# Optimization experiments

Hardware: AMD Instinct MI355X
Metric: run time of the kernel (lower is better)

The kernel has to match this reference:

```python
import jax, jax.numpy as jnp
import numpy as np

L, N, E, H = 4096, 1, 1024, 16
DH = E // H
SCALE = DH ** -0.5


def setup_inputs() -> dict:
    key = jax.random.key(0)
    k1, k2, k3 = jax.random.split(key, 3)
    # xavier_uniform-ish scales for faithfulness of magnitude
    lim_qkv = (6.0 / (3 * E + E)) ** 0.5
    lim_out = (6.0 / (E + E)) ** 0.5
    x = jax.random.normal(k1, (L, N, E), dtype=jnp.float32)
    w_qkv = jax.random.uniform(k2, (3 * E, E), dtype=jnp.float32, minval=-lim_qkv, maxval=lim_qkv)
    w_out = jax.random.uniform(k3, (E, E), dtype=jnp.float32, minval=-lim_out, maxval=lim_out)
    return {"x": x, "w_qkv": w_qkv, "w_out": w_out}


def reference(x, w_qkv, w_out):
    # x: [L, N, E]
    qkv = jnp.einsum('lne,fe->lnf', x, w_qkv)          # [L, N, 3E]
    q, k, v = jnp.split(qkv, 3, axis=-1)               # each [L, N, E]

    def to_heads(t):
        # [L, N, E] -> [N*H, L, DH]
        return t.reshape(L, N * H, DH).transpose(1, 0, 2)

    q = to_heads(q) * SCALE
    k = to_heads(k)
    v = to_heads(v)
    attn = jnp.einsum('bld,bmd->blm', q, k)            # [N*H, L, L]
    attn = jax.nn.softmax(attn, axis=-1)
    out = jnp.einsum('blm,bmd->bld', attn, v)          # [N*H, L, DH]
    out = out.transpose(1, 0, 2).reshape(L, N, E)
    return jnp.einsum('lne,fe->lnf', out, w_out)       # [L, N, E]
```

## Files before the change

### kernel.cpp

```cpp
#include <hip/hip_runtime.h>
#include <hip/hip_bf16.h>
#include <stdint.h>

#define L_SEQ 4096
#define EMB   1024
#define NHEAD 16
#define DHEAD 64

#define SM_SCALE 0.18033688011112042f
#define SM_FIXED_MAX 12.0f

typedef __attribute__((ext_vector_type(8))) short short8;
typedef __attribute__((ext_vector_type(4))) short s16x4;
typedef __attribute__((ext_vector_type(4))) float f32x4;

struct Pack8 { f32x4 lo, hi; };

__device__ inline short f2bf(float f) {
  union { float f; unsigned u; } c; c.f = f;
  unsigned r = (c.u + 0x7fffu + ((c.u >> 16) & 1u)) >> 16;
  return (short)(unsigned short)r;
}
__device__ inline unsigned fbits(float f) {
  union { float f; unsigned u; } c; c.f = f; return c.u;
}
__device__ inline unsigned pack_trunc(float f0, float f1) {
#if __has_builtin(__builtin_amdgcn_perm)
  return __builtin_amdgcn_perm(fbits(f1), fbits(f0), 0x07060302u);
#else
  return (fbits(f0) >> 16) | (fbits(f1) & 0xffff0000u);
#endif
}

#if __has_builtin(__builtin_amdgcn_exp2f)
#define EXP2F(x) __builtin_amdgcn_exp2f(x)
#else
#define EXP2F(x) exp2f(x)
#endif

__device__ inline void pl16swap(unsigned &x, unsigned &y) {
#if __has_builtin(__builtin_amdgcn_permlane16_swap)
  auto r = __builtin_amdgcn_permlane16_swap(x, y, false, false);
  x = r[0]; y = r[1];
#else
  asm volatile("v_permlane16_swap_b32 %0, %1" : "+v"(x), "+v"(y));
#endif
}

__device__ inline short8 mk8(unsigned d0, unsigned d1, unsigned d2, unsigned d3) {
  union { unsigned u[4]; short8 s; } c;
  c.u[0] = d0; c.u[1] = d1; c.u[2] = d2; c.u[3] = d3;
  return c.s;
}

template<bool F32>
__device__ inline auto ld8(const void* p, size_t off) {
  if constexpr (F32) {
    const float* f = (const float*)p + off;
    Pack8 r; r.lo = *(const f32x4*)f; r.hi = *(const f32x4*)(f + 4);
    return r;
  } else {
    return *(const short8*)((const short*)p + off);
  }
}
__device__ inline short8 cvt8(Pack8 r) {
  short8 o;
#pragma unroll
  for (int j = 0; j < 4; ++j) { o[j] = f2bf(r.lo[j]); o[4 + j] = f2bf(r.hi[j]); }
  return o;
}
__device__ inline short8 cvt8(short8 r) { return r; }

#define MFMA16(a, b, c) __builtin_amdgcn_mfma_f32_16x16x32_bf16(a, b, c, 0, 0, 0)
#define FZERO ((f32x4){0.f, 0.f, 0.f, 0.f})

__device__ inline void stage16(const void* g, void* l) {
  __builtin_amdgcn_global_load_lds(
      (const __attribute__((address_space(1))) void*)g,
      (__attribute__((address_space(3))) void*)l, 16, 0, 0);
}

__global__ __launch_bounds__(256)
void conv_kernel(const float* __restrict__ in, short* __restrict__ out, int n) {
  int i = (blockIdx.x * 256 + threadIdx.x) * 8;
  if (i >= n) return;
  Pack8 r; r.lo = *(const f32x4*)(in + i); r.hi = *(const f32x4*)(in + i + 4);
  *(short8*)(out + i) = cvt8(r);
}

__global__ __launch_bounds__(256, 3)
void gemm_qkv_dma(const short* __restrict__ A, const short* __restrict__ B,
                  short* __restrict__ qb, short* __restrict__ kb,
                  short* __restrict__ vt) {
  __shared__ __align__(16) short At[128 * 32];
  __shared__ __align__(16) short Bt[128 * 32];

  const int tid  = threadIdx.x;
  const int lane = tid & 63;
  const int wave = tid >> 6;
  const int quad = lane >> 4;
  const int l15  = lane & 15;
  const int q8   = quad << 3;

  const int bm  = (blockIdx.x / 24) << 7;
  const int bn  = (blockIdx.x % 24) << 7;
  const int wr  = wave >> 1;
  const int wc  = wave & 1;

  const short* Ab = A + (size_t)bm * EMB;
  const short* Bb = B + (size_t)bn * EMB;

  f32x4 acc[4][4];
#pragma unroll
  for (int r = 0; r < 4; ++r)
#pragma unroll
    for (int c = 0; c < 4; ++c) acc[r][c] = FZERO;

  const int arow = (wr * 64 + l15) * 32 + q8;
  const int brow = (wc * 64 + l15) * 32 + q8;
  const int wbase = tid & ~63;

  for (int kt = 0; kt < 32; ++kt) {
    __syncthreads();
    const int k0 = kt << 5;
#pragma unroll
    for (int j = 0; j < 2; ++j) {
      const int s = j * 256 + tid;
      const int row = s >> 2, qc = (s & 3) << 3;
      stage16(Ab + (size_t)row * EMB + k0 + qc,
              At + (size_t)(j * 256 + wbase) * 8);
      stage16(Bb + (size_t)row * EMB + k0 + qc,
              Bt + (size_t)(j * 256 + wbase) * 8);
    }
    __syncthreads();

    short8 af[4], bf[4];
#pragma unroll
    for (int r = 0; r < 4; ++r) af[r] = *(const short8*)(At + arow + r * 512);
#pragma unroll
    for (int c = 0; c < 4; ++c) bf[c] = *(const short8*)(Bt + brow + c * 512);
#pragma unroll
    for (int r = 0; r < 4; ++r)
#pragma unroll
      for (int c = 0; c < 4; ++c)
        acc[r][c] = MFMA16(af[r], bf[c], acc[r][c]);
  }

  if (bn < 2048) {
    short* dst = (bn < 1024) ? qb : kb;
    const int bcol = (bn < 1024) ? bn : bn - 1024;
    const float cs = (bn < 1024) ? SM_SCALE : 1.0f;
#pragma unroll
    for (int r = 0; r < 4; ++r)
#pragma unroll
      for (int c = 0; c < 4; ++c) {
        const int col = bcol + wc * 64 + c * 16 + l15;
#pragma unroll
        for (int reg = 0; reg < 4; ++reg) {
          const int row = bm + wr * 64 + r * 16 + quad * 4 + reg;
          dst[(size_t)row * EMB + col] = f2bf(acc[r][c][reg] * cs);
        }
      }
  } else {
    const int bcol = bn - 2048;
#pragma unroll
    for (int r = 0; r < 4; ++r)
#pragma unroll
      for (int c = 0; c < 4; ++c) {
        const int col  = bcol + wc * 64 + c * 16 + l15;
        const int rowb = bm + wr * 64 + r * 16 + quad * 4;
        s16x4 pk;
#pragma unroll
        for (int reg = 0; reg < 4; ++reg) pk[reg] = f2bf(acc[r][c][reg]);
        *(s16x4*)(vt + (size_t)col * L_SEQ + rowb) = pk;
      }
  }
}

__global__ __launch_bounds__(256, 3)
void gemm_qkv_f32(const short* __restrict__ A, const float* __restrict__ B,
                  short* __restrict__ qb, short* __restrict__ kb,
                  short* __restrict__ vt) {
  __shared__ __align__(16) short At[128 * 40];
  __shared__ __align__(16) short Bt[128 * 40];

  const int tid  = threadIdx.x;
  const int lane = tid & 63;
  const int wave = tid >> 6;
  const int quad = lane >> 4;
  const int l15  = lane & 15;
  const int q8   = quad << 3;

  const int bm  = (blockIdx.x / 24) << 7;
  const int bn  = (blockIdx.x % 24) << 7;
  const int wr  = wave >> 1;
  const int wc  = wave & 1;

  const int s0 = tid, s1 = tid + 256;
  const int ar0 = s0 >> 2, ac0 = (s0 & 3) << 3;
  const int ar1 = s1 >> 2, ac1 = (s1 & 3) << 3;

  const size_t aoff0 = (size_t)(bm + ar0) * EMB + ac0;
  const size_t aoff1 = (size_t)(bm + ar1) * EMB + ac1;
  const size_t boff0 = (size_t)(bn + ar0) * EMB + ac0;
  const size_t boff1 = (size_t)(bn + ar1) * EMB + ac1;

  f32x4 acc[4][4];
#pragma unroll
  for (int r = 0; r < 4; ++r)
#pragma unroll
    for (int c = 0; c < 4; ++c) acc[r][c] = FZERO;

  short8 ga0 = *(const short8*)(A + aoff0);
  short8 ga1 = *(const short8*)(A + aoff1);
  Pack8  gb0 = ld8<true>(B, boff0);
  Pack8  gb1 = ld8<true>(B, boff1);

  const int arow = (wr * 64 + l15) * 40 + q8;
  const int brow = (wc * 64 + l15) * 40 + q8;

  for (int kt = 0; kt < 32; ++kt) {
    __syncthreads();
    *(short8*)(At + ar0 * 40 + ac0) = ga0;
    *(short8*)(At + ar1 * 40 + ac1) = ga1;
    *(short8*)(Bt + ar0 * 40 + ac0) = cvt8(gb0);
    *(short8*)(Bt + ar1 * 40 + ac1) = cvt8(gb1);
    __syncthreads();

    if (kt + 1 < 32) {
      const size_t k0 = (size_t)(kt + 1) << 5;
      ga0 = *(const short8*)(A + aoff0 + k0);
      ga1 = *(const short8*)(A + aoff1 + k0);
      gb0 = ld8<true>(B, boff0 + k0);
      gb1 = ld8<true>(B, boff1 + k0);
    }

    short8 af[4], bf[4];
#pragma unroll
    for (int r = 0; r < 4; ++r) af[r] = *(const short8*)(At + arow + r * 640);
#pragma unroll
    for (int c = 0; c < 4; ++c) bf[c] = *(const short8*)(Bt + brow + c * 640);
#pragma unroll
    for (int r = 0; r < 4; ++r)
#pragma unroll
      for (int c = 0; c < 4; ++c)
        acc[r][c] = MFMA16(af[r], bf[c], acc[r][c]);
  }

  if (bn < 2048) {
    short* dst = (bn < 1024) ? qb : kb;
    const int bcol = (bn < 1024) ? bn : bn - 1024;
    const float cs = (bn < 1024) ? SM_SCALE : 1.0f;
#pragma unroll
    for (int r = 0; r < 4; ++r)
#pragma unroll
      for (int c = 0; c < 4; ++c) {
        const int col = bcol + wc * 64 + c * 16 + l15;
#pragma unroll
        for (int reg = 0; reg < 4; ++reg) {
          const int row = bm + wr * 64 + r * 16 + quad * 4 + reg;
          dst[(size_t)row * EMB + col] = f2bf(acc[r][c][reg] * cs);
        }
      }
  } else {
    const int bcol = bn - 2048;
#pragma unroll
    for (int r = 0; r < 4; ++r)
#pragma unroll
      for (int c = 0; c < 4; ++c) {
        const int col  = bcol + wc * 64 + c * 16 + l15;
        const int rowb = bm + wr * 64 + r * 16 + quad * 4;
        s16x4 pk;
#pragma unroll
        for (int reg = 0; reg < 4; ++reg) pk[reg] = f2bf(acc[r][c][reg]);
        *(s16x4*)(vt + (size_t)col * L_SEQ + rowb) = pk;
      }
  }
}

__global__ __launch_bounds__(256, 3)
void gemm_out_dma(const short* __restrict__ A, const short* __restrict__ B,
                  float* __restrict__ C) {
  __shared__ __align__(16) short At[128 * 32];
  __shared__ __align__(16) short Bt[64 * 32];

  const int tid  = threadIdx.x;
  const int lane = tid & 63;
  const int wave = tid >> 6;
  const int quad = lane >> 4;
  const int l15  = lane & 15;
  const int q8   = quad << 3;

  const int bm  = (blockIdx.x >> 4) << 7;
  const int bn  = (blockIdx.x & 15) << 6;
  const int wr  = wave >> 1;
  const int wc  = wave & 1;

  const short* Ab = A + (size_t)bm * EMB;
  const short* Bb = B + (size_t)bn * EMB;

  f32x4 acc[4][2];
#pragma unroll
  for (int r = 0; r < 4; ++r)
#pragma unroll
    for (int c = 0; c < 2; ++c) acc[r][c] = FZERO;

  const int arow = (wr * 64 + l15) * 32 + q8;
  const int brow = (wc * 32 + l15) * 32 + q8;
  const int wbase = tid & ~63;

  for (int kt = 0; kt < 32; ++kt) {
    __syncthreads();
    const int k0 = kt << 5;
#pragma unroll
    for (int j = 0; j < 2; ++j) {
      const int s = j * 256 + tid;
      const int row = s >> 2, qc = (s & 3) << 3;
      stage16(Ab + (size_t)row * EMB + k0 + qc,
              At + (size_t)(j * 256 + wbase) * 8);
    }
    {
      const int row = tid >> 2, qc = (tid & 3) << 3;
      stage16(Bb + (size_t)row * EMB + k0 + qc, Bt + (size_t)wbase * 8);
    }
    __syncthreads();

    short8 af[4], bf[2];
#pragma unroll
    for (int r = 0; r < 4; ++r) af[r] = *(const short8*)(At + arow + r * 512);
#pragma unroll
    for (int c = 0; c < 2; ++c) bf[c] = *(const short8*)(Bt + brow + c * 512);
#pragma unroll
    for (int r = 0; r < 4; ++r)
#pragma unroll
      for (int c = 0; c < 2; ++c)
        acc[r][c] = MFMA16(af[r], bf[c], acc[r][c]);
  }

#pragma unroll
  for (int r = 0; r < 4; ++r) {
#pragma unroll
    for (int c = 0; c < 2; ++c) {
      const int col = bn + wc * 32 + c * 16 + l15;
#pragma unroll
      for (int reg = 0; reg < 4; ++reg) {
        const int row = bm + wr * 64 + r * 16 + quad * 4 + reg;
        C[(size_t)row * EMB + col] = acc[r][c][reg];
      }
    }
  }
}

__global__ __launch_bounds__(256, 3)
void attn_kernel(short* __restrict__ qo, const short* __restrict__ kbuf,
                 const short* __restrict__ vtbuf) {
  __shared__ __align__(16) short SH[4][64 * 64];

  const int tid  = threadIdx.x;
  const int lane = tid & 63;
  const int w    = tid >> 6;
  const int quad = lane >> 4;
  const int l15  = lane & 15;
  const int q8   = quad << 3;
  const int vb   = ((quad & 1) << 4) | ((quad >> 1) << 3);

  const int h    = blockIdx.x >> 5;
  const int qblk = blockIdx.x & 31;
  const int hcol = h * 64;

  short8 qf[2][2];
#pragma unroll
  for (int g = 0; g < 2; ++g) {
    const short* qp = qo + (size_t)(qblk * 128 + w * 32 + g * 16 + l15) * EMB + hcol;
    qf[g][0] = *(const short8*)(qp + q8);
    qf[g][1] = *(const short8*)(qp + 32 + q8);
  }

  const short8 vone = {0x3F80, 0x3F80, 0x3F80, 0x3F80,
                       0x3F80, 0x3F80, 0x3F80, 0x3F80};

  f32x4 o[2][4];
#pragma unroll
  for (int g = 0; g < 2; ++g)
#pragma unroll
    for (int f = 0; f < 4; ++f) o[g][f] = FZERO;
  f32x4 l_c[2] = {FZERO, FZERO};

  const int r0  = tid >> 3;
  const int lc8 = ((tid & 7) ^ (r0 & 7)) << 3;
  const short* kp0 = kbuf + (size_t)r0 * EMB + hcol + lc8;
  const short* kp1 = kp0 + (size_t)32 * EMB;
  const short* vp0 = vtbuf + (size_t)(hcol + r0) * L_SEQ + lc8;
  const short* vp1 = vp0 + (size_t)32 * L_SEQ;
  const int d0 = (tid & ~63) * 8;
  const int d1 = 2048 + d0;

  const int sx8 = (l15 & 7) << 3;
  const int pk0 = q8 ^ sx8, pk1 = pk0 ^ 32;
  const int pv0 = vb ^ sx8, pv1 = pv0 ^ 32;

  stage16(kp0, &SH[0][0] + d0);
  stage16(kp1, &SH[0][0] + d1);
  stage16(vp0, &SH[2][0] + d0);
  stage16(vp1, &SH[2][0] + d1);

  for (int t = 0; t < 64; ++t) {
    short* const ktb = &SH[t & 1][0];
    short* const vtb = &SH[2 + (t & 1)][0];

    __syncthreads();

    if (t < 63) {
      const size_t ko = (size_t)(t + 1) * 64 * EMB;
      const size_t vo = (size_t)(t + 1) * 64;
      short* const kd = &SH[(t + 1) & 1][0];
      short* const vd = &SH[2 + ((t + 1) & 1)][0];
      stage16(kp0 + ko, kd + d0);
      stage16(kp1 + ko, kd + d1);
      stage16(vp0 + vo, vd + d0);
      stage16(vp1 + vo, vd + d1);
    }

    f32x4 s[2][4];
#pragma unroll
    for (int f = 0; f < 4; ++f) {
      const int krow = (f * 16 + l15) * 64;
      short8 kf0 = *(const short8*)(ktb + krow + pk0);
      short8 kf1 = *(const short8*)(ktb + krow + pk1);
      s[0][f] = MFMA16(kf0, qf[0][0], FZERO);
      s[0][f] = MFMA16(kf1, qf[0][1], s[0][f]);
      s[1][f] = MFMA16(kf0, qf[1][0], FZERO);
      s[1][f] = MFMA16(kf1, qf[1][1], s[1][f]);
    }

    short8 pa[2][2];
#pragma unroll
    for (int g = 0; g < 2; ++g) {
      float p[4][4];
#pragma unroll
      for (int f = 0; f < 4; ++f)
#pragma unroll
        for (int r = 0; r < 4; ++r)
          p[f][r] = EXP2F(s[g][f][r] - SM_FIXED_MAX);

      unsigned pk[4][2];
#pragma unroll
      for (int f = 0; f < 4; ++f) {
        pk[f][0] = pack_trunc(p[f][0], p[f][1]);
        pk[f][1] = pack_trunc(p[f][2], p[f][3]);
      }
      pl16swap(pk[0][0], pk[1][0]);
      pl16swap(pk[0][1], pk[1][1]);
      pl16swap(pk[2][0], pk[3][0]);
      pl16swap(pk[2][1], pk[3][1]);
      pa[g][0] = mk8(pk[0][0], pk[0][1], pk[1][0], pk[1][1]);
      pa[g][1] = mk8(pk[2][0], pk[2][1], pk[3][0], pk[3][1]);

      f32x4 rsv = MFMA16(pa[g][0], vone, FZERO);
      rsv = MFMA16(pa[g][1], vone, rsv);
#pragma unroll
      for (int r = 0; r < 4; ++r) l_c[g][r] += rsv[r];
    }

#pragma unroll
    for (int f = 0; f < 4; ++f) {
      const int vrow = (f * 16 + l15) * 64;
      short8 v0 = *(const short8*)(vtb + vrow + pv0);
      short8 v1 = *(const short8*)(vtb + vrow + pv1);
      o[0][f] = MFMA16(pa[0][0], v0, o[0][f]);
      o[0][f] = MFMA16(pa[0][1], v1, o[0][f]);
      o[1][f] = MFMA16(pa[1][0], v0, o[1][f]);
      o[1][f] = MFMA16(pa[1][1], v1, o[1][f]);
    }
  }

  __syncthreads();
  short* const pw = &SH[0][0] + w * (32 * 72);
#pragma unroll
  for (int g = 0; g < 2; ++g) {
    f32x4 inv;
#pragma unroll
    for (int r = 0; r < 4; ++r) inv[r] = 1.0f / l_c[g][r];
    short* const pg = pw + g * (16 * 72);
#pragma unroll
    for (int f = 0; f < 4; ++f)
#pragma unroll
      for (int r = 0; r < 4; ++r)
        pg[(quad * 4 + r) * 72 + f * 16 + l15] = f2bf(o[g][f][r] * inv[r]);
  }

#pragma unroll
  for (int rr = 0; rr < 4; ++rr) {
    const int row = (lane >> 3) + rr * 8;
    const int c8  = (lane & 7) << 3;
    short8 gv = *(const short8*)(pw + row * 72 + c8);
    *(short8*)(qo + (size_t)(qblk * 128 + w * 32 + row) * EMB + hcol + c8) = gv;
  }
}

extern "C" void kernel_launch(void* const* d_in, const int* in_sizes, int n_in,
                              void* d_out, int out_size, void* d_ws, size_t ws_size,
                              hipStream_t stream) {
  (void)in_sizes; (void)n_in; (void)out_size;
  const float* x     = (const float*)d_in[0];
  const float* w_qkv = (const float*)d_in[1];
  const float* w_out = (const float*)d_in[2];

  short* qbuf  = (short*)d_ws;
  short* x_bf  = qbuf + (size_t)L_SEQ * EMB;
  short* wo_bf = x_bf;
  short* wq_bf = x_bf + (size_t)L_SEQ * EMB;
  short* kbuf  = (short*)d_out;
  short* vtbuf = kbuf + (size_t)L_SEQ * EMB;
  float* outp  = (float*)d_out;

  const bool big_ws = ws_size >= (size_t)24 * 1024 * 1024;

  conv_kernel<<<dim3(L_SEQ * EMB / 2048), 256, 0, stream>>>(x, x_bf, L_SEQ * EMB);
  if (big_ws)
    conv_kernel<<<dim3(3 * EMB * EMB / 2048), 256, 0, stream>>>(w_qkv, wq_bf, 3 * EMB * EMB);

  if (big_ws)
    gemm_qkv_dma<<<dim3(768), 256, 0, stream>>>(x_bf, wq_bf, qbuf, kbuf, vtbuf);
  else
    gemm_qkv_f32<<<dim3(768), 256, 0, stream>>>(x_bf, w_qkv, qbuf, kbuf, vtbuf);

  conv_kernel<<<dim3(EMB * EMB / 2048), 256, 0, stream>>>(w_out, wo_bf, EMB * EMB);

  attn_kernel<<<dim3(NHEAD * (L_SEQ / 128)), 256, 0, stream>>>(qbuf, kbuf, vtbuf);

  gemm_out_dma<<<dim3(512), 256, 0, stream>>>(qbuf, wo_bf, outp);
}
```

Before: 217.0 us.

## Double KV tile to 128 keys per iteration with chunked inner loop

The attention loop now stages 128-key K and V^T tiles per iteration instead of 64, which halves the number of barriers and loop iterations. Each tile is processed in four 32-key chunks, so the score and P registers stay small. The V^T shared-memory swizzle is widened to 16 chunks to match the new 128-column rows. Occupancy is lowered from 3 to 2 blocks per CU because each block now uses twice the LDS.

```diff
diff --git a/kernel.cpp b/kernel.cpp
--- a/kernel.cpp
+++ b/kernel.cpp
@@ -351,10 +351,10 @@
   }
 }
 
-__global__ __launch_bounds__(256, 3)
+__global__ __launch_bounds__(256, 2)
 void attn_kernel(short* __restrict__ qo, const short* __restrict__ kbuf,
                  const short* __restrict__ vtbuf) {
-  __shared__ __align__(16) short SH[4][64 * 64];
+  __shared__ __align__(16) short SH[4][128 * 64];
 
   const int tid  = threadIdx.x;
   const int lane = tid & 63;
@@ -362,7 +362,7 @@
   const int quad = lane >> 4;
   const int l15  = lane & 15;
   const int q8   = quad << 3;
-  const int vb   = ((quad & 1) << 4) | ((quad >> 1) << 3);
+  const int vb8  = ((quad & 1) << 1) | (quad >> 1);
 
   const int h    = blockIdx.x >> 5;
   const int qblk = blockIdx.x & 31;
@@ -386,91 +386,93 @@
     for (int f = 0; f < 4; ++f) o[g][f] = FZERO;
   f32x4 l_c[2] = {FZERO, FZERO};
 
-  const int r0  = tid >> 3;
-  const int lc8 = ((tid & 7) ^ (r0 & 7)) << 3;
-  const short* kp0 = kbuf + (size_t)r0 * EMB + hcol + lc8;
-  const short* kp1 = kp0 + (size_t)32 * EMB;
-  const short* vp0 = vtbuf + (size_t)(hcol + r0) * L_SEQ + lc8;
-  const short* vp1 = vp0 + (size_t)32 * L_SEQ;
-  const int d0 = (tid & ~63) * 8;
-  const int d1 = 2048 + d0;
-
-  const int sx8 = (l15 & 7) << 3;
-  const int pk0 = q8 ^ sx8, pk1 = pk0 ^ 32;
-  const int pv0 = vb ^ sx8, pv1 = pv0 ^ 32;
-
-  stage16(kp0, &SH[0][0] + d0);
-  stage16(kp1, &SH[0][0] + d1);
-  stage16(vp0, &SH[2][0] + d0);
-  stage16(vp1, &SH[2][0] + d1);
-
-  for (int t = 0; t < 64; ++t) {
+  const int kr0  = tid >> 3;
+  const int klc8 = ((tid & 7) ^ (kr0 & 7)) << 3;
+  const int vr0  = tid >> 4;
+  const int vlc8 = ((tid & 15) ^ vr0) << 3;
+  const short* kp = kbuf + (size_t)kr0 * EMB + hcol + klc8;
+  const short* vp = vtbuf + (size_t)(hcol + vr0) * L_SEQ + vlc8;
+  const int db = (tid & ~63) * 8;
+
+  const int sx7 = (l15 & 7) << 3;
+  const int pk0 = q8 ^ sx7, pk1 = pk0 ^ 32;
+
+#pragma unroll
+  for (int jj = 0; jj < 4; ++jj) {
+    stage16(kp + (size_t)jj * 32 * EMB,  &SH[0][0] + jj * 2048 + db);
+    stage16(vp + (size_t)jj * 16 * L_SEQ, &SH[2][0] + jj * 2048 + db);
+  }
+
+  for (int t = 0; t < 32; ++t) {
     short* const ktb = &SH[t & 1][0];
     short* const vtb = &SH[2 + (t & 1)][0];
 
     __syncthreads();
 
-    if (t < 63) {
-      const size_t ko = (size_t)(t + 1) * 64 * EMB;
-      const size_t vo = (size_t)(t + 1) * 64;
+    if (t < 31) {
+      const short* kpt = kp + (size_t)(t + 1) * 128 * EMB;
+      const short* vpt = vp + (size_t)(t + 1) * 128;
       short* const kd = &SH[(t + 1) & 1][0];
       short* const vd = &SH[2 + ((t + 1) & 1)][0];
-      stage16(kp0 + ko, kd + d0);
-      stage16(kp1 + ko, kd + d1);
-      stage16(vp0 + vo, vd + d0);
-      stage16(vp1 + vo, vd + d1);
-    }
-
-    f32x4 s[2][4];
-#pragma unroll
-    for (int f = 0; f < 4; ++f) {
-      const int krow = (f * 16 + l15) * 64;
-      short8 kf0 = *(const short8*)(ktb + krow + pk0);
-      short8 kf1 = *(const short8*)(ktb + krow + pk1);
-      s[0][f] = MFMA16(kf0, qf[0][0], FZERO);
-      s[0][f] = MFMA16(kf1, qf[0][1], s[0][f]);
-      s[1][f] = MFMA16(kf0, qf[1][0], FZERO);
-      s[1][f] = MFMA16(kf1, qf[1][1], s[1][f]);
-    }
-
-    short8 pa[2][2];
-#pragma unroll
-    for (int g = 0; g < 2; ++g) {
-      float p[4][4];
-#pragma unroll
-      for (int f = 0; f < 4; ++f)
-#pragma unroll
-        for (int r = 0; r < 4; ++r)
-          p[f][r] = EXP2F(s[g][f][r] - SM_FIXED_MAX);
-
-      unsigned pk[4][2];
-#pragma unroll
-      for (int f = 0; f < 4; ++f) {
-        pk[f][0] = pack_trunc(p[f][0], p[f][1]);
-        pk[f][1] = pack_trunc(p[f][2], p[f][3]);
-      }
-      pl16swap(pk[0][0], pk[1][0]);
-      pl16swap(pk[0][1], pk[1][1]);
-      pl16swap(pk[2][0], pk[3][0]);
-      pl16swap(pk[2][1], pk[3][1]);
-      pa[g][0] = mk8(pk[0][0], pk[0][1], pk[1][0], pk[1][1]);
-      pa[g][1] = mk8(pk[2][0], pk[2][1], pk[3][0], pk[3][1]);
-
-      f32x4 rsv = MFMA16(pa[g][0], vone, FZERO);
-      rsv = MFMA16(pa[g][1], vone, rsv);
-#pragma unroll
-      for (int r = 0; r < 4; ++r) l_c[g][r] += rsv[r];
-    }
-
-#pragma unroll
-    for (int f = 0; f < 4; ++f) {
-      const int vrow = (f * 16 + l15) * 64;
-      short8 v0 = *(const short8*)(vtb + vrow + pv0);
-      short8 v1 = *(const short8*)(vtb + vrow + pv1);
-      o[0][f] = MFMA16(pa[0][0], v0, o[0][f]);
-      o[0][f] = MFMA16(pa[0][1], v1, o[0][f]);
-      o[1][f] = MFMA16(pa[1][0], v0, o[1][f]);
-      o[1][f] = MFMA16(pa[1][1], v1, o[1][f]);
+#pragma unroll
+      for (int jj = 0; jj < 4; ++jj) {
+        stage16(kpt + (size_t)jj * 32 * EMB,  kd + jj * 2048 + db);
+        stage16(vpt + (size_t)jj * 16 * L_SEQ, vd + jj * 2048 + db);
+      }
+    }
+
+#pragma unroll
+    for (int j = 0; j < 4; ++j) {
+      const int kra = (j * 32 + l15) * 64;
+      const int krb = (j * 32 + 16 + l15) * 64;
+      short8 kf0a = *(const short8*)(ktb + kra + pk0);
+      short8 kf0b = *(const short8*)(ktb + kra + pk1);
+      short8 kf1a = *(const short8*)(ktb + krb + pk0);
+      short8 kf1b = *(const short8*)(ktb + krb + pk1);
+
+      f32x4 s[2][2];
+      s[0][0] = MFMA16(kf0a, qf[0][0], FZERO);
+      s[0][0] = MFMA16(kf0b, qf[0][1], s[0][0]);
+      s[0][1] = MFMA16(kf1a, qf[0][0], FZERO);
+      s[0][1] = MFMA16(kf1b, qf[0][1], s[0][1]);
+      s[1][0] = MFMA16(kf0a, qf[1][0], FZERO);
+      s[1][0] = MFMA16(kf0b, qf[1][1], s[1][0]);
+      s[1][1] = MFMA16(kf1a, qf[1][0], FZERO);
+      s[1][1] = MFMA16(kf1b, qf[1][1], s[1][1]);
+
+      short8 pa[2];
+#pragma unroll
+      for (int g = 0; g < 2; ++g) {
+        float p[2][4];
+#pragma unroll
+        for (int i = 0; i < 2; ++i)
+#pragma unroll
+          for (int r = 0; r < 4; ++r)
+            p[i][r] = EXP2F(s[g][i][r] - SM_FIXED_MAX);
+
+        unsigned pk[2][2];
+#pragma unroll
+        for (int i = 0; i < 2; ++i) {
+          pk[i][0] = pack_trunc(p[i][0], p[i][1]);
+          pk[i][1] = pack_trunc(p[i][2], p[i][3]);
+        }
+        pl16swap(pk[0][0], pk[1][0]);
+        pl16swap(pk[0][1], pk[1][1]);
+        pa[g] = mk8(pk[0][0], pk[0][1], pk[1][0], pk[1][1]);
+
+        f32x4 rsv = MFMA16(pa[g], vone, FZERO);
+#pragma unroll
+        for (int r = 0; r < 4; ++r) l_c[g][r] += rsv[r];
+      }
+
+#pragma unroll
+      for (int fd = 0; fd < 4; ++fd) {
+        const int vrow = (fd * 16 + l15) * 128;
+        const int pc   = (((j << 2) | vb8) ^ l15) << 3;
+        short8 vf = *(const short8*)(vtb + vrow + pc);
+        o[0][fd] = MFMA16(pa[0], vf, o[0][fd]);
+        o[1][fd] = MFMA16(pa[1], vf, o[1][fd]);
+      }
     }
   }
 
```

New measurement: 211.8 us. -2.4%, faster.
